# Kernel optimization log

Measured on AMD Instinct MI355X. Metric: run time of the kernel, lower is better.

The kernel has to match this reference:

```python
import jax, jax.numpy as jnp
import numpy as np

C = 64            # irrep multiplicity (64x0e + 64x1o)
N_BASIS = 8
N_SPECIES = 5
AVG_NEIGH = 16.0
CUTOFF = 5.0
N_PATHS = 5       # (0e*Y0->0e),(0e*Y1->1o),(1o*Y0->1o),(1o.Y1->0e),(1o x Y1->1)


def setup_inputs() -> dict:
    key = jax.random.key(0)
    ks = jax.random.split(key, 16)
    N, E = 20000, 320000
    def w(k, shape, fan_in):
        return jax.random.normal(k, shape, dtype=jnp.float32) / jnp.sqrt(jnp.float32(fan_in))
    return {
        "vectors": jax.random.normal(ks[0], (E, 3), dtype=jnp.float32),
        "node_feats": jax.random.normal(ks[1], (N, 4 * C), dtype=jnp.float32),
        "node_specie": jax.random.randint(ks[2], (N,), 0, N_SPECIES),
        "senders": jax.random.randint(ks[3], (E,), 0, N),
        "receivers": jax.random.randint(ks[4], (E,), 0, N),
        # linear_up (per-irrep channel mixing)
        "W0_up": w(ks[5], (C, C), C),
        "W1_up": w(ks[6], (C, C), C),
        # radial MLP: 8 -> 64 -> 64 -> 5*C
        "Wm1": w(ks[7], (N_BASIS, 64), N_BASIS),
        "Wm2": w(ks[8], (64, 64), 64),
        "Wm3": w(ks[9], (64, N_PATHS * C), 64),
        # skip_tp: species-indexed linear to 128x0e + 64x1o
        "Ws0": w(ks[10], (N_SPECIES, C, 2 * C), C),
        "Ws1": w(ks[11], (N_SPECIES, C, C), C),
        # linear_down: messages irreps -> 128x0e + 64x1o
        "Wd0": w(ks[12], (C, 2 * C), C),
        "Wd1": w(ks[13], (C, C), C),
    }


def reference(vectors, node_feats, node_specie, senders, receivers,
              W0_up, W1_up, Wm1, Wm2, Wm3, Ws0, Ws1, Wd0, Wd1):
    N = node_feats.shape[0]
    E = vectors.shape[0]
    x0 = node_feats[:, :C]                       # [N,C]   0e scalars
    x1 = node_feats[:, C:].reshape(N, C, 3)      # [N,C,3] 1o vectors

    # linear_up then gather by senders
    u0 = x0 @ W0_up
    u1 = jnp.einsum('nci,cd->ndi', x1, W1_up)
    m0 = u0[senders]                             # [E,C]
    m1 = u1[senders]                             # [E,C,3]

    # radial basis (bessel) and edge-weight MLP
    r = jnp.linalg.norm(vectors, axis=-1, keepdims=True)   # [E,1]
    safe_r = jnp.where(r == 0.0, 1.0, r)
    Y1 = vectors / safe_r                                  # [E,3] unit direction (l=1 SH)
    n = jnp.arange(1, N_BASIS + 1, dtype=vectors.dtype)
    basis = jnp.sqrt(2.0 / CUTOFF) * jnp.sin(n * jnp.pi * r / CUTOFF) / safe_r  # [E,8]
    h = jax.nn.silu(basis @ Wm1)
    h = jax.nn.silu(h @ Wm2)
    wmix = h @ Wm3                                         # [E, 5*C]
    wmix = jnp.where(r == 0.0, 0.0, wmix)                  # zero weights at zero-length edges
    w00, w01, w10, w11d, w11c = jnp.split(wmix, N_PATHS, axis=-1)  # each [E,C]

    # per-edge equivariant tensor product (LinearSHTP, l<=1 CG paths)
    dot = jnp.einsum('eci,ei->ec', m1, Y1)                 # 1o . Y1 -> scalar
    crs = jnp.cross(m1, Y1[:, None, :])                    # 1o x Y1 -> vector
    msg0 = w00 * m0 + w11d * dot                           # [E,C]
    msg1 = (w01 * m0)[..., None] * Y1[:, None, :] \
           + w10[..., None] * m1 + w11c[..., None] * crs   # [E,C,3]

    # scatter_sum to receivers, normalize by sqrt(avg_num_neighbors)
    inv = 1.0 / jnp.sqrt(jnp.float32(AVG_NEIGH))
    a0 = jax.ops.segment_sum(msg0, receivers, num_segments=N) * inv
    a1 = jax.ops.segment_sum(msg1.reshape(E, 3 * C), receivers, num_segments=N).reshape(N, C, 3) * inv

    # linear_down to 128x0e + 64x1o (extra 0e scalars are the gates)
    d0 = a0 @ Wd0                                          # [N,2C]
    d1 = jnp.einsum('nci,cd->ndi', a1, Wd1)                # [N,C,3]

    # skip_tp: species-indexed linear on original node features
    s0 = jnp.einsum('nc,ncd->nd', x0, Ws0[node_specie])    # [N,2C]
    s1 = jnp.einsum('nci,ncd->ndi', x1, Ws1[node_specie])  # [N,C,3]

    f0 = d0 + s0
    f1 = d1 + s1

    # gate: first C scalars -> even_act(silu); next C scalars gate the 1o vectors
    scalars = jax.nn.silu(f0[:, :C])
    gates = jax.nn.silu(f0[:, C:])
    vec = f1 * gates[..., None]
    return jnp.concatenate([scalars, vec.reshape(N, 3 * C)], axis=-1)  # [N, 4C]
```

## Files before the change

### kernel.cpp

```cpp
#include <hip/hip_runtime.h>
#include <hip/hip_bf16.h>

typedef __attribute__((ext_vector_type(8))) short short8;
typedef __attribute__((ext_vector_type(4))) float f32x4;
typedef __attribute__((ext_vector_type(4))) unsigned short us4v;

__device__ __forceinline__ unsigned bf16u(float x) {
    unsigned u = __float_as_uint(x);
    return (u + 0x7fffu + ((u >> 16) & 1u)) >> 16;
}
__device__ __forceinline__ short bf16s(float x) { return (short)bf16u(x); }

__global__ __launch_bounds__(256) void prep_kernel(
    const float* __restrict__ Wm1, const float* __restrict__ Wm2,
    const float* __restrict__ Wm3,
    const float* __restrict__ Wd0, const float* __restrict__ Ws0,
    const float* __restrict__ Wd1, const float* __restrict__ Ws1,
    short* __restrict__ W1B, short* __restrict__ Wm2B, short* __restrict__ W3B,
    short* __restrict__ WoB, int* __restrict__ cnt, int N)
{
    const int tid = blockIdx.x * 256 + threadIdx.x;
    const int nth = gridDim.x * 256;

    for (int i = tid; i < N * 16; i += nth) cnt[i] = 0;

    for (int idx = tid; idx < 52 * 64; idx += nth) {
        int l = idx & 63, f = idx >> 6;
        int g = l >> 4, c = l & 15;
        short8 v;
        if (f < 4) {
            #pragma unroll
            for (int i = 0; i < 8; ++i)
                v[i] = (g == 0) ? bf16s(Wm1[(size_t)i * 64 + f * 16 + c]) : (short)0;
            *(short8*)(W1B + (size_t)f * 512 + l * 8) = v;
        } else if (f < 12) {
            int f2 = f - 4, t = f2 >> 1, kh = f2 & 1;
            #pragma unroll
            for (int i = 0; i < 8; ++i)
                v[i] = bf16s(Wm2[(size_t)(kh * 32 + g * 8 + i) * 64 + t * 16 + c]);
            *(short8*)(Wm2B + (size_t)f2 * 512 + l * 8) = v;
        } else {
            int f3 = f - 12, t = f3 >> 1, kh = f3 & 1;
            #pragma unroll
            for (int i = 0; i < 8; ++i)
                v[i] = bf16s(Wm3[(size_t)(kh * 32 + g * 8 + i) * 320 + t * 16 + c]);
            *(short8*)(W3B + (size_t)f3 * 512 + l * 8) = v;
        }
    }

    for (int idx = tid; idx < 144 * 64; idx += nth) {
        int l = idx & 63, f = idx >> 6;
        int g = l >> 4, c = l & 15;
        short8 v;
        if (f < 16) {
            int t = f >> 1, kh = f & 1;
            #pragma unroll
            for (int i = 0; i < 8; ++i)
                v[i] = bf16s(Wd0[(size_t)(kh * 32 + g * 8 + i) * 128 + t * 16 + c]);
        } else if (f < 96) {
            int s = (f - 16) >> 4, r = (f - 16) & 15, t = r >> 1, kh = r & 1;
            #pragma unroll
            for (int i = 0; i < 8; ++i)
                v[i] = bf16s(Ws0[((size_t)s * 64 + kh * 32 + g * 8 + i) * 128 + t * 16 + c]);
        } else if (f < 104) {
            int r = f - 96, t = r >> 1, kh = r & 1;
            #pragma unroll
            for (int i = 0; i < 8; ++i)
                v[i] = bf16s(Wd1[(size_t)(kh * 32 + g * 8 + i) * 64 + t * 16 + c]);
        } else {
            int s = (f - 104) >> 3, r = (f - 104) & 7, t = r >> 1, kh = r & 1;
            #pragma unroll
            for (int i = 0; i < 8; ++i)
                v[i] = bf16s(Ws1[((size_t)s * 64 + kh * 32 + g * 8 + i) * 64 + t * 16 + c]);
        }
        *(short8*)(WoB + (size_t)f * 512 + l * 8) = v;
    }
}

__global__ __launch_bounds__(256) void rank_kernel(
    const int* __restrict__ receivers, int* __restrict__ cnt,
    int* __restrict__ rank, int E)
{
    int i = blockIdx.x * 256 + threadIdx.x;
    int stride = gridDim.x * 256;
    for (; i < E; i += stride)
        rank[i] = atomicAdd(&cnt[receivers[i] << 4], 1);
}

__global__ __launch_bounds__(256) void scan1_kernel(
    const int* __restrict__ cnt, int* __restrict__ offs,
    int* __restrict__ part, int N)
{
    __shared__ int a_[256], b_[256];
    const int b = blockIdx.x, t = threadIdx.x;
    const int base = b * 1024 + t * 4;
    int v[4];
    #pragma unroll
    for (int k = 0; k < 4; ++k)
        v[k] = (base + k < N) ? cnt[(size_t)(base + k) << 4] : 0;
    int sum = v[0] + v[1] + v[2] + v[3];
    a_[t] = sum;
    __syncthreads();
    int* src = a_; int* dst = b_;
    for (int off = 1; off < 256; off <<= 1) {
        dst[t] = src[t] + ((t >= off) ? src[t - off] : 0);
        __syncthreads();
        int* tmp = src; src = dst; dst = tmp;
    }
    int excl = src[t] - sum;
    if (t == 0) part[b] = src[255];
    int run = excl;
    #pragma unroll
    for (int k = 0; k < 4; ++k) {
        if (base + k < N) offs[base + k] = run;
        run += v[k];
    }
}

__global__ __launch_bounds__(256) void scan23_kernel(
    int* __restrict__ offs, const int* __restrict__ part, int nblk, int N)
{
    __shared__ int base_s, total_s;
    const int b = blockIdx.x, t = threadIdx.x;
    if (t == 0) {
        int s = 0, tot = 0;
        for (int i = 0; i < nblk; ++i) {
            if (i < b) s += part[i];
            tot += part[i];
        }
        base_s = s; total_s = tot;
    }
    __syncthreads();
    const int add = base_s;
    const int base = b * 1024 + t * 4;
    #pragma unroll
    for (int k = 0; k < 4; ++k) {
        int i = base + k;
        if (i < N) offs[i] += add;
    }
    if (b == 0 && t == 0) offs[N] = total_s;
}

__global__ __launch_bounds__(256) void fpnu_kernel(
    const float* __restrict__ vectors, const int* __restrict__ senders,
    const int* __restrict__ receivers, const int* __restrict__ offs,
    const int* __restrict__ rank,
    uint4* __restrict__ epackA, float4* __restrict__ epackB,
    const float* __restrict__ node_feats, const float* __restrict__ W0_up,
    const float* __restrict__ W1_up, uint2* __restrict__ ubf,
    short* __restrict__ xpk, int E, int N, int FPB)
{
    __shared__ float lnf[4][256];
    if (blockIdx.x < FPB) {
        int i = blockIdx.x * 256 + threadIdx.x;
        int stride = FPB * 256;
        for (; i < E; i += stride) {
            int pos = offs[receivers[i]] + rank[i];
            float vx = vectors[3 * (size_t)i + 0];
            float vy = vectors[3 * (size_t)i + 1];
            float vz = vectors[3 * (size_t)i + 2];
            float r = sqrtf(vx * vx + vy * vy + vz * vz);
            float ir = (r != 0.f) ? 1.f / r : 0.f;
            float ang = r * 0.6283185307179586f;
            float s1, c1;
            __sincosf(ang, &s1, &c1);
            float tc = 2.f * c1;
            float sb = s1, sp = 0.f;
            float coef = 0.6324555320336759f * ir;
            unsigned bw[4];
            #pragma unroll
            for (int h = 0; h < 4; ++h) {
                unsigned lo = bf16u(sb * coef);
                float nx = tc * sb - sp; sp = sb; sb = nx;
                unsigned hi = bf16u(sb * coef);
                nx = tc * sb - sp; sp = sb; sb = nx;
                bw[h] = lo | (hi << 16);
            }
            epackA[pos] = make_uint4(bw[0], bw[1], bw[2], bw[3]);
            epackB[pos] = make_float4(vx * ir, vy * ir, vz * ir,
                                      __int_as_float(senders[i]));
        }
    } else {
        const int wv = threadIdx.x >> 6;
        const int d  = threadIdx.x & 63;
        int nb = (blockIdx.x - FPB) * 4 + wv;
        if (nb >= N) return;

        float4 v4 = *(const float4*)(node_feats + (size_t)nb * 256 + d * 4);
        *(float4*)&lnf[wv][d * 4] = v4;

        float a0 = 0.f, ax = 0.f, ay = 0.f, az = 0.f;
        #pragma unroll 8
        for (int cc = 0; cc < 64; ++cc) {
            float w0 = W0_up[cc * 64 + d];
            float w1 = W1_up[cc * 64 + d];
            float x0v = lnf[wv][cc];
            float xxv = lnf[wv][64 + cc * 3 + 0];
            float xyv = lnf[wv][64 + cc * 3 + 1];
            float xzv = lnf[wv][64 + cc * 3 + 2];
            a0 += x0v * w0;
            ax += xxv * w1;
            ay += xyv * w1;
            az += xzv * w1;
        }
        ubf[(size_t)nb * 64 + d] = make_uint2(bf16u(a0) | (bf16u(ax) << 16),
                                              bf16u(ay) | (bf16u(az) << 16));
        short* xp = xpk + (size_t)nb * 256;
        xp[d]       = bf16s(lnf[wv][d]);
        xp[64 + d]  = bf16s(lnf[wv][64 + d * 3 + 0]);
        xp[128 + d] = bf16s(lnf[wv][64 + d * 3 + 1]);
        xp[192 + d] = bf16s(lnf[wv][64 + d * 3 + 2]);
    }
}

__global__ __launch_bounds__(256) void mlp_kernel(
    const uint4* __restrict__ epackA,
    const short* __restrict__ W1B, const short* __restrict__ Wm2B,
    const short* __restrict__ W3B, unsigned short* __restrict__ wmix,
    int P, int nwaves)
{
    __shared__ __align__(16) short ldsW3[40 * 512];
    __shared__ __align__(16) short ldsH[4][1024];

    {
        const short8* src = (const short8*)W3B;
        short8* dst = (short8*)ldsW3;
        for (int i = threadIdx.x; i < 2560; i += 256) dst[i] = src[i];
    }
    __syncthreads();

    const int lane = threadIdx.x & 63;
    const int wv   = threadIdx.x >> 6;
    const int gw   = blockIdx.x * 4 + wv;
    const int c = lane & 15, g = lane >> 4;
    const int nwin = (P + 15) >> 4;

    for (int w = gw; w < nwin; w += nwaves) {
        const int p0 = w << 4;

        short8 basisA = {0, 0, 0, 0, 0, 0, 0, 0};
        if (lane < 16) {
            uint4 ba = epackA[p0 + lane];
            union { uint4 u4v; short8 s8; } cv;
            cv.u4v = ba;
            basisA = cv.s8;
        }

        #pragma unroll
        for (int t = 0; t < 4; ++t) {
            f32x4 h = {0.f, 0.f, 0.f, 0.f};
            short8 bf = *(const short8*)(W1B + (size_t)t * 512 + lane * 8);
            h = __builtin_amdgcn_mfma_f32_16x16x32_bf16(basisA, bf, h, 0, 0, 0);
            #pragma unroll
            for (int i = 0; i < 4; ++i) {
                float x = h[i];
                float h1 = x / (1.f + __expf(-x));
                int row = 4 * g + i;
                ldsH[wv][row * 64 + ((16 * t + c) ^ ((row & 7) << 3))] = bf16s(h1);
            }
        }
        short8 h1f0 = *(const short8*)&ldsH[wv][c * 64 + ((g * 8) ^ ((c & 7) << 3))];
        short8 h1f1 = *(const short8*)&ldsH[wv][c * 64 + ((32 + g * 8) ^ ((c & 7) << 3))];

        #pragma unroll
        for (int t = 0; t < 4; ++t) {
            f32x4 h = {0.f, 0.f, 0.f, 0.f};
            short8 b0 = *(const short8*)(Wm2B + (size_t)(t * 2) * 512 + lane * 8);
            short8 b1 = *(const short8*)(Wm2B + (size_t)(t * 2 + 1) * 512 + lane * 8);
            h = __builtin_amdgcn_mfma_f32_16x16x32_bf16(h1f0, b0, h, 0, 0, 0);
            h = __builtin_amdgcn_mfma_f32_16x16x32_bf16(h1f1, b1, h, 0, 0, 0);
            #pragma unroll
            for (int i = 0; i < 4; ++i) {
                float x = h[i];
                float h2 = x / (1.f + __expf(-x));
                int row = 4 * g + i;
                ldsH[wv][row * 64 + ((16 * t + c) ^ ((row & 7) << 3))] = bf16s(h2);
            }
        }
        short8 h2f0 = *(const short8*)&ldsH[wv][c * 64 + ((g * 8) ^ ((c & 7) << 3))];
        short8 h2f1 = *(const short8*)&ldsH[wv][c * 64 + ((32 + g * 8) ^ ((c & 7) << 3))];

        unsigned short* wbase = wmix + (size_t)w * 5120 + lane * 4;
        #pragma unroll
        for (int t = 0; t < 20; ++t) {
            f32x4 wq = {0.f, 0.f, 0.f, 0.f};
            short8 b0 = *(const short8*)(ldsW3 + (size_t)(t * 2) * 512 + lane * 8);
            short8 b1 = *(const short8*)(ldsW3 + (size_t)(t * 2 + 1) * 512 + lane * 8);
            wq = __builtin_amdgcn_mfma_f32_16x16x32_bf16(h2f0, b0, wq, 0, 0, 0);
            wq = __builtin_amdgcn_mfma_f32_16x16x32_bf16(h2f1, b1, wq, 0, 0, 0);
            us4v st;
            #pragma unroll
            for (int i = 0; i < 4; ++i) st[i] = (unsigned short)bf16u(wq[i]);
            *(us4v*)(wbase + t * 256) = st;
        }
    }
}

__global__ __launch_bounds__(256) void gather_kernel(
    const float4* __restrict__ epackB, const int* __restrict__ offs,
    const uint2* __restrict__ ubf, const unsigned short* __restrict__ wmix,
    float* __restrict__ acc, int N)
{
    const int lane = threadIdx.x & 63;
    const int n = blockIdx.x * 4 + (threadIdx.x >> 6);
    if (n >= N) return;
    const int q = lane >> 4, c = lane & 15;

    const int beg = offs[n], end = offs[n + 1];
    float a0 = 0.f, a1x = 0.f, a1y = 0.f, a1z = 0.f;

    for (int base = beg & ~3; base < end; base += 4) {
        const unsigned short* wn = wmix
            + (size_t)(base >> 4) * 5120
            + (q << 8) + (((base & 15) >> 2) << 6) + (c << 2);
        us4v wp0 = *(const us4v*)(wn);
        us4v wp1 = *(const us4v*)(wn + 1024);
        us4v wp2 = *(const us4v*)(wn + 2048);
        us4v wp3 = *(const us4v*)(wn + 3072);
        us4v wp4 = *(const us4v*)(wn + 4096);

        #pragma unroll
        for (int i = 0; i < 4; ++i) {
            int pos = base + i;
            bool valid = (pos >= beg) && (pos < end);
            float4 mb = epackB[pos];
            int snd = valid ? __float_as_int(mb.w) : 0;
            uint2 mu = ubf[(size_t)snd * 64 + lane];
            float w00  = valid ? __uint_as_float((unsigned)wp0[i] << 16) : 0.f;
            float w01  = valid ? __uint_as_float((unsigned)wp1[i] << 16) : 0.f;
            float w10  = valid ? __uint_as_float((unsigned)wp2[i] << 16) : 0.f;
            float w11d = valid ? __uint_as_float((unsigned)wp3[i] << 16) : 0.f;
            float w11c = valid ? __uint_as_float((unsigned)wp4[i] << 16) : 0.f;
            float m0  = __uint_as_float(mu.x << 16);
            float m1x = __uint_as_float(mu.x & 0xffff0000u);
            float m1y = __uint_as_float(mu.y << 16);
            float m1z = __uint_as_float(mu.y & 0xffff0000u);

            float dotv = m1x * mb.x + m1y * mb.y + m1z * mb.z;
            a0 += w00 * m0 + w11d * dotv;
            float wm = w01 * m0;
            a1x += wm * mb.x + w10 * m1x + w11c * (m1y * mb.z - m1z * mb.y);
            a1y += wm * mb.y + w10 * m1y + w11c * (m1z * mb.x - m1x * mb.z);
            a1z += wm * mb.z + w10 * m1z + w11c * (m1x * mb.y - m1y * mb.x);
        }
    }

    float* ar = acc + (size_t)n * 256;
    ar[lane]       = a0;
    ar[64 + lane]  = a1x;
    ar[128 + lane] = a1y;
    ar[192 + lane] = a1z;
}

__global__ __launch_bounds__(256) void edge_kernel(
    const uint4* __restrict__ epackA, const float4* __restrict__ epackB,
    const int* __restrict__ offs, const uint2* __restrict__ ubf,
    const short* __restrict__ W1B, const short* __restrict__ Wm2B,
    const short* __restrict__ W3B, float* __restrict__ acc,
    int N, int nwaves)
{
    __shared__ __align__(16) short ldsW3[40 * 512];
    __shared__ __align__(16) short ldsH[4][1024];
    __shared__ __align__(16) float ldsMeta[4][16][4];

    {
        const short8* src = (const short8*)W3B;
        short8* dst = (short8*)ldsW3;
        for (int i = threadIdx.x; i < 2560; i += 256) dst[i] = src[i];
    }
    __syncthreads();

    const int lane = threadIdx.x & 63;
    const int wv   = threadIdx.x >> 6;
    const int gw   = blockIdx.x * 4 + wv;
    const int c = lane & 15, g = lane >> 4;

    for (int n = gw; n < N; n += nwaves) {
        float a0q[4]  = {0.f, 0.f, 0.f, 0.f};
        float a1xq[4] = {0.f, 0.f, 0.f, 0.f};
        float a1yq[4] = {0.f, 0.f, 0.f, 0.f};
        float a1zq[4] = {0.f, 0.f, 0.f, 0.f};
        const int beg = offs[n], end = offs[n + 1];

        for (int p0 = beg; p0 < end; p0 += 16) {
            const int m = end - p0;
            short8 basisA = {0, 0, 0, 0, 0, 0, 0, 0};
            if (lane < 16) {
                uint4 ba = epackA[p0 + lane];
                float4 mb = epackB[p0 + lane];
                if (lane >= m) {
                    ba = make_uint4(0u, 0u, 0u, 0u);
                    mb = make_float4(0.f, 0.f, 0.f, __int_as_float(0));
                }
                union { uint4 u4v; short8 s8; } cv;
                cv.u4v = ba;
                basisA = cv.s8;
                *(float4*)&ldsMeta[wv][lane][0] = mb;
            }
            float Yx[4], Yy[4], Yz[4];
            int snd[4];
            #pragma unroll
            for (int i = 0; i < 4; ++i) {
                float4 mt = *(const float4*)&ldsMeta[wv][4 * g + i][0];
                Yx[i] = mt.x; Yy[i] = mt.y; Yz[i] = mt.z;
                snd[i] = __float_as_int(mt.w);
            }

#define PFETCH(Q, MV)                                                       \
            _Pragma("unroll")                                               \
            for (int i = 0; i < 4; ++i)                                     \
                MV[i] = ubf[(size_t)snd[i] * 64 + 16 * (Q) + c];

#define COMPQ(Q, MV)                                                        \
        {                                                                   \
            float M0[4], M1X[4], M1Y[4], M1Z[4];                            \
            _Pragma("unroll")                                               \
            for (int i = 0; i < 4; ++i) {                                   \
                M0[i]  = __uint_as_float(MV[i].x << 16);                    \
                M1X[i] = __uint_as_float(MV[i].x & 0xffff0000u);            \
                M1Y[i] = __uint_as_float(MV[i].y << 16);                    \
                M1Z[i] = __uint_as_float(MV[i].y & 0xffff0000u);            \
            }                                                               \
            _Pragma("unroll")                                               \
            for (int p = 0; p < 5; ++p) {                                   \
                const int t = 4 * p + (Q);                                  \
                f32x4 w = {0.f, 0.f, 0.f, 0.f};                             \
                short8 b0 = *(const short8*)(ldsW3 + (size_t)(t * 2) * 512 + lane * 8);     \
                short8 b1 = *(const short8*)(ldsW3 + (size_t)(t * 2 + 1) * 512 + lane * 8); \
                w = __builtin_amdgcn_mfma_f32_16x16x32_bf16(h2f0, b0, w, 0, 0, 0);          \
                w = __builtin_amdgcn_mfma_f32_16x16x32_bf16(h2f1, b1, w, 0, 0, 0);          \
                _Pragma("unroll")                                           \
                for (int i = 0; i < 4; ++i) {                               \
                    float wv_ = w[i];                                       \
                    if (p == 0) {                                           \
                        a0q[Q] += wv_ * M0[i];                              \
                    } else if (p == 1) {                                    \
                        float tt = wv_ * M0[i];                             \
                        a1xq[Q] += tt * Yx[i];                              \
                        a1yq[Q] += tt * Yy[i];                              \
                        a1zq[Q] += tt * Yz[i];                              \
                    } else if (p == 2) {                                    \
                        a1xq[Q] += wv_ * M1X[i];                            \
                        a1yq[Q] += wv_ * M1Y[i];                            \
                        a1zq[Q] += wv_ * M1Z[i];                            \
                    } else if (p == 3) {                                    \
                        a0q[Q] += wv_ * (M1X[i] * Yx[i] + M1Y[i] * Yy[i] + M1Z[i] * Yz[i]); \
                    } else {                                                \
                        a1xq[Q] += wv_ * (M1Y[i] * Yz[i] - M1Z[i] * Yy[i]); \
                        a1yq[Q] += wv_ * (M1Z[i] * Yx[i] - M1X[i] * Yz[i]); \
                        a1zq[Q] += wv_ * (M1X[i] * Yy[i] - M1Y[i] * Yx[i]); \
                    }                                                       \
                }                                                           \
            }                                                               \
        }

            uint2 mA[4], mB[4];
            PFETCH(0, mA);
            PFETCH(1, mB);
            __builtin_amdgcn_sched_barrier(0);

            #pragma unroll
            for (int t = 0; t < 4; ++t) {
                f32x4 h = {0.f, 0.f, 0.f, 0.f};
                short8 bf = *(const short8*)(W1B + (size_t)t * 512 + lane * 8);
                h = __builtin_amdgcn_mfma_f32_16x16x32_bf16(basisA, bf, h, 0, 0, 0);
                #pragma unroll
                for (int i = 0; i < 4; ++i) {
                    float x = h[i];
                    float h1 = x / (1.f + __expf(-x));
                    int row = 4 * g + i;
                    ldsH[wv][row * 64 + ((16 * t + c) ^ ((row & 7) << 3))] = bf16s(h1);
                }
            }
            short8 h1f0 = *(const short8*)&ldsH[wv][c * 64 + ((g * 8) ^ ((c & 7) << 3))];
            short8 h1f1 = *(const short8*)&ldsH[wv][c * 64 + ((32 + g * 8) ^ ((c & 7) << 3))];

            #pragma unroll
            for (int t = 0; t < 4; ++t) {
                f32x4 h = {0.f, 0.f, 0.f, 0.f};
                short8 b0 = *(const short8*)(Wm2B + (size_t)(t * 2) * 512 + lane * 8);
                short8 b1 = *(const short8*)(Wm2B + (size_t)(t * 2 + 1) * 512 + lane * 8);
                h = __builtin_amdgcn_mfma_f32_16x16x32_bf16(h1f0, b0, h, 0, 0, 0);
                h = __builtin_amdgcn_mfma_f32_16x16x32_bf16(h1f1, b1, h, 0, 0, 0);
                #pragma unroll
                for (int i = 0; i < 4; ++i) {
                    float x = h[i];
                    float h2 = x / (1.f + __expf(-x));
                    int row = 4 * g + i;
                    ldsH[wv][row * 64 + ((16 * t + c) ^ ((row & 7) << 3))] = bf16s(h2);
                }
            }
            short8 h2f0 = *(const short8*)&ldsH[wv][c * 64 + ((g * 8) ^ ((c & 7) << 3))];
            short8 h2f1 = *(const short8*)&ldsH[wv][c * 64 + ((32 + g * 8) ^ ((c & 7) << 3))];

            COMPQ(0, mA);
            __builtin_amdgcn_sched_barrier(0);
            PFETCH(2, mA);
            COMPQ(1, mB);
            __builtin_amdgcn_sched_barrier(0);
            PFETCH(3, mB);
            COMPQ(2, mA);
            __builtin_amdgcn_sched_barrier(0);
            COMPQ(3, mB);
#undef PFETCH
#undef COMPQ
        }

        #pragma unroll
        for (int q = 0; q < 4; ++q) {
            a0q[q]  += __shfl_xor(a0q[q], 16);  a0q[q]  += __shfl_xor(a0q[q], 32);
            a1xq[q] += __shfl_xor(a1xq[q], 16); a1xq[q] += __shfl_xor(a1xq[q], 32);
            a1yq[q] += __shfl_xor(a1yq[q], 16); a1yq[q] += __shfl_xor(a1yq[q], 32);
            a1zq[q] += __shfl_xor(a1zq[q], 16); a1zq[q] += __shfl_xor(a1zq[q], 32);
        }
        if (lane < 16) {
            float* ar = acc + (size_t)n * 256;
            #pragma unroll
            for (int q = 0; q < 4; ++q) {
                ar[16 * q + lane]       = a0q[q];
                ar[64 + 16 * q + lane]  = a1xq[q];
                ar[128 + 16 * q + lane] = a1yq[q];
                ar[192 + 16 * q + lane] = a1zq[q];
            }
        }
    }
}

__global__ __launch_bounds__(256) void node_out_kernel(
    const float* __restrict__ acc, const short* __restrict__ xpk,
    const int* __restrict__ node_specie, const short* __restrict__ WoB,
    float* __restrict__ out, int N)
{
    __shared__ float ldsOut[4][16][256];
    const int lane = threadIdx.x & 63;
    const int wv   = threadIdx.x >> 6;
    const int c = lane & 15, g = lane >> 4;
    const int n0 = (blockIdx.x * 4 + wv) * 16;
    if (n0 >= N) return;

    const int nc = min(n0 + c, N - 1);
    const int sp_c = node_specie[nc];
    const short8 z8 = {0, 0, 0, 0, 0, 0, 0, 0};

    short8 x0f[2], a0hi[2], a0lo[2];
    #pragma unroll
    for (int kh = 0; kh < 2; ++kh) {
        x0f[kh] = *(const short8*)&xpk[(size_t)nc * 256 + kh * 32 + g * 8];
        const float* ap = acc + (size_t)nc * 256 + kh * 32 + g * 8;
        #pragma unroll
        for (int i = 0; i < 8; ++i) {
            float v = 0.25f * ap[i];
            unsigned h = bf16u(v);
            a0hi[kh][i] = (short)h;
            a0lo[kh][i] = (short)bf16u(v - __uint_as_float(h << 16));
        }
    }

    f32x4 w0[8];
    #pragma unroll
    for (int t = 0; t < 8; ++t) w0[t] = (f32x4){0.f, 0.f, 0.f, 0.f};
    #pragma unroll
    for (int t = 0; t < 8; ++t)
        #pragma unroll
        for (int kh = 0; kh < 2; ++kh) {
            short8 b = *(const short8*)(WoB + (size_t)(t * 2 + kh) * 512 + lane * 8);
            w0[t] = __builtin_amdgcn_mfma_f32_16x16x32_bf16(a0hi[kh], b, w0[t], 0, 0, 0);
            w0[t] = __builtin_amdgcn_mfma_f32_16x16x32_bf16(a0lo[kh], b, w0[t], 0, 0, 0);
        }
    #pragma unroll
    for (int s = 0; s < 5; ++s) {
        if (!__any(sp_c == s)) continue;
        short8 mk0 = (sp_c == s) ? x0f[0] : z8;
        short8 mk1 = (sp_c == s) ? x0f[1] : z8;
        #pragma unroll
        for (int t = 0; t < 8; ++t) {
            short8 b0 = *(const short8*)(WoB + (size_t)(16 + s * 16 + t * 2) * 512 + lane * 8);
            short8 b1 = *(const short8*)(WoB + (size_t)(16 + s * 16 + t * 2 + 1) * 512 + lane * 8);
            w0[t] = __builtin_amdgcn_mfma_f32_16x16x32_bf16(mk0, b0, w0[t], 0, 0, 0);
            w0[t] = __builtin_amdgcn_mfma_f32_16x16x32_bf16(mk1, b1, w0[t], 0, 0, 0);
        }
    }
    float gate[4][4];
    #pragma unroll
    for (int t = 0; t < 8; ++t)
        #pragma unroll
        for (int i = 0; i < 4; ++i) {
            float x = w0[t][i];
            float sv = x / (1.f + __expf(-x));
            if (t < 4) ldsOut[wv][4 * g + i][16 * t + c] = sv;
            else       gate[t - 4][i] = sv;
        }

    short8 x1f[3][2], a1hi[3][2], a1lo[3][2];
    #pragma unroll
    for (int j = 0; j < 3; ++j)
        #pragma unroll
        for (int kh = 0; kh < 2; ++kh) {
            x1f[j][kh] = *(const short8*)&xpk[(size_t)nc * 256 + (1 + j) * 64 + kh * 32 + g * 8];
            const float* ap = acc + (size_t)nc * 256 + 64 + 64 * j + kh * 32 + g * 8;
            #pragma unroll
            for (int i = 0; i < 8; ++i) {
                float v = 0.25f * ap[i];
                unsigned h = bf16u(v);
                a1hi[j][kh][i] = (short)h;
                a1lo[j][kh][i] = (short)bf16u(v - __uint_as_float(h << 16));
            }
        }

    f32x4 w1[3][4];
    #pragma unroll
    for (int j = 0; j < 3; ++j)
        #pragma unroll
        for (int t = 0; t < 4; ++t) w1[j][t] = (f32x4){0.f, 0.f, 0.f, 0.f};
    #pragma unroll
    for (int t = 0; t < 4; ++t)
        #pragma unroll
        for (int kh = 0; kh < 2; ++kh) {
            short8 b = *(const short8*)(WoB + (size_t)(96 + t * 2 + kh) * 512 + lane * 8);
            #pragma unroll
            for (int j = 0; j < 3; ++j) {
                w1[j][t] = __builtin_amdgcn_mfma_f32_16x16x32_bf16(a1hi[j][kh], b, w1[j][t], 0, 0, 0);
                w1[j][t] = __builtin_amdgcn_mfma_f32_16x16x32_bf16(a1lo[j][kh], b, w1[j][t], 0, 0, 0);
            }
        }
    #pragma unroll
    for (int s = 0; s < 5; ++s) {
        if (!__any(sp_c == s)) continue;
        short8 m1[3][2];
        #pragma unroll
        for (int j = 0; j < 3; ++j) {
            m1[j][0] = (sp_c == s) ? x1f[j][0] : z8;
            m1[j][1] = (sp_c == s) ? x1f[j][1] : z8;
        }
        #pragma unroll
        for (int t = 0; t < 4; ++t)
            #pragma unroll
            for (int kh = 0; kh < 2; ++kh) {
                short8 b = *(const short8*)(WoB + (size_t)(104 + s * 8 + t * 2 + kh) * 512 + lane * 8);
                #pragma unroll
                for (int j = 0; j < 3; ++j)
                    w1[j][t] = __builtin_amdgcn_mfma_f32_16x16x32_bf16(m1[j][kh], b, w1[j][t], 0, 0, 0);
            }
    }
    #pragma unroll
    for (int j = 0; j < 3; ++j)
        #pragma unroll
        for (int t = 0; t < 4; ++t)
            #pragma unroll
            for (int i = 0; i < 4; ++i)
                ldsOut[wv][4 * g + i][64 + (16 * t + c) * 3 + j] = w1[j][t][i] * gate[t][i];

    #pragma unroll 4
    for (int r = 0; r < 16; ++r) {
        int nn = n0 + r;
        if (nn < N)
            *(float4*)&out[(size_t)nn * 256 + lane * 4] =
                *(const float4*)&ldsOut[wv][r][lane * 4];
    }
}

extern "C" void kernel_launch(void* const* d_in, const int* in_sizes, int n_in,
                              void* d_out, int out_size, void* d_ws, size_t ws_size,
                              hipStream_t stream) {
    const float* vectors     = (const float*)d_in[0];
    const float* node_feats  = (const float*)d_in[1];
    const int*   node_specie = (const int*)d_in[2];
    const int*   senders     = (const int*)d_in[3];
    const int*   receivers   = (const int*)d_in[4];
    const float* W0_up       = (const float*)d_in[5];
    const float* W1_up       = (const float*)d_in[6];
    const float* Wm1         = (const float*)d_in[7];
    const float* Wm2         = (const float*)d_in[8];
    const float* Wm3         = (const float*)d_in[9];
    const float* Ws0         = (const float*)d_in[10];
    const float* Ws1         = (const float*)d_in[11];
    const float* Wd0         = (const float*)d_in[12];
    const float* Wd1         = (const float*)d_in[13];
    float* out = (float*)d_out;

    int E = in_sizes[0] / 3;
    int N = in_sizes[1] / 256;
    int nblk = (N + 1023) / 1024;

    char* wp = (char*)d_ws;
    uint2* ubf     = (uint2*)wp;                wp += (size_t)N * 64 * 8;
    float* acc     = (float*)wp;                wp += (size_t)N * 256 * 4;
    short* xpk     = (short*)wp;                wp += (size_t)N * 256 * 2;
    uint4* epackA  = (uint4*)wp;                wp += (size_t)(E + 16) * 16;
    float4* epackB = (float4*)wp;               wp += (size_t)(E + 16) * 16;
    unsigned short* wmix = (unsigned short*)wp;
    size_t wmix_bytes = (size_t)(E + 16) * 320 * 2;
    size_t base_used = (size_t)(wp - (char*)d_ws);
    size_t other_bytes = (4 + 8 + 40 + 144) * 512 * 2
                       + (size_t)N * 16 * 4
                       + (size_t)(N + 1) * 4
                       + (size_t)E * 4
                       + (size_t)(nblk + 1) * 4 + 256;
    bool use_split = (base_used + wmix_bytes + other_bytes) <= ws_size;
    if (use_split) wp += wmix_bytes;

    short* W1B    = (short*)wp;                 wp += 4 * 512 * 2;
    short* Wm2B   = (short*)wp;                 wp += 8 * 512 * 2;
    short* W3B    = (short*)wp;                 wp += 40 * 512 * 2;
    short* WoB    = (short*)wp;                 wp += 144 * 512 * 2;
    int*   cnt    = (int*)wp;                   wp += (size_t)N * 16 * 4;
    int*   offs   = (int*)wp;                   wp += (size_t)(N + 1) * 4;
    int*   rank   = (int*)wp;                   wp += (size_t)E * 4;
    int*   part   = (int*)wp;                   wp += (size_t)(nblk + 1) * 4;

    prep_kernel<<<80, 256, 0, stream>>>(
        Wm1, Wm2, Wm3, Wd0, Ws0, Wd1, Ws1, W1B, Wm2B, W3B, WoB, cnt, N);
    rank_kernel<<<1024, 256, 0, stream>>>(receivers, cnt, rank, E);
    scan1_kernel<<<nblk, 256, 0, stream>>>(cnt, offs, part, N);
    scan23_kernel<<<nblk, 256, 0, stream>>>(offs, part, nblk, N);
    const int FPB = 1024;
    fpnu_kernel<<<FPB + (N + 3) / 4, 256, 0, stream>>>(
        vectors, senders, receivers, offs, rank, epackA, epackB,
        node_feats, W0_up, W1_up, ubf, xpk, E, N, FPB);

    if (use_split) {
        mlp_kernel<<<768, 256, 0, stream>>>(
            epackA, W1B, Wm2B, W3B, wmix, E, 768 * 4);
        gather_kernel<<<(N + 3) / 4, 256, 0, stream>>>(
            epackB, offs, ubf, wmix, acc, N);
    } else {
        edge_kernel<<<512, 256, 0, stream>>>(
            epackA, epackB, offs, ubf, W1B, Wm2B, W3B, acc, N, 512 * 4);
    }

    int ngroups = (N + 15) / 16;
    node_out_kernel<<<(ngroups + 3) / 4, 256, 0, stream>>>(
        acc, xpk, node_specie, WoB, out, N);
}
```

Baseline: 205.1 us.

## Pad per-node edge segments to multiples of four for aligned gather

The CSR scan now rounds each node's degree up to a multiple of 4, so every node's edge segment starts on a 4-aligned position. The gather loop can start at beg directly and drops the lower-bound validity check, and the end is taken from the real count. The MLP reads the padded total from the device instead of using E, and the edge buffers grow by up to 3N entries. The trade-off is extra MLP work on padding slots, more memory, and reliance on the padding entries being harmless (they are masked by the valid check).

```diff
diff --git a/kernel.cpp b/kernel.cpp
--- a/kernel.cpp
+++ b/kernel.cpp
@@ -96,8 +96,10 @@
     const int base = b * 1024 + t * 4;
     int v[4];
     #pragma unroll
-    for (int k = 0; k < 4; ++k)
-        v[k] = (base + k < N) ? cnt[(size_t)(base + k) << 4] : 0;
+    for (int k = 0; k < 4; ++k) {
+        int d = (base + k < N) ? cnt[(size_t)(base + k) << 4] : 0;
+        v[k] = (d + 3) & ~3;
+    }
     int sum = v[0] + v[1] + v[2] + v[3];
     a_[t] = sum;
     __syncthreads();
@@ -214,10 +216,10 @@
 }
 
 __global__ __launch_bounds__(256) void mlp_kernel(
-    const uint4* __restrict__ epackA,
+    const uint4* __restrict__ epackA, const int* __restrict__ totalp,
     const short* __restrict__ W1B, const short* __restrict__ Wm2B,
     const short* __restrict__ W3B, unsigned short* __restrict__ wmix,
-    int P, int nwaves)
+    int nwaves)
 {
     __shared__ __align__(16) short ldsW3[40 * 512];
     __shared__ __align__(16) short ldsH[4][1024];
@@ -229,6 +231,7 @@
     }
     __syncthreads();
 
+    const int P = *totalp;
     const int lane = threadIdx.x & 63;
     const int wv   = threadIdx.x >> 6;
     const int gw   = blockIdx.x * 4 + wv;
@@ -298,6 +301,7 @@
 
 __global__ __launch_bounds__(256) void gather_kernel(
     const float4* __restrict__ epackB, const int* __restrict__ offs,
+    const int* __restrict__ cnt,
     const uint2* __restrict__ ubf, const unsigned short* __restrict__ wmix,
     float* __restrict__ acc, int N)
 {
@@ -306,10 +310,12 @@
     if (n >= N) return;
     const int q = lane >> 4, c = lane & 15;
 
-    const int beg = offs[n], end = offs[n + 1];
+    const int beg = offs[n];
+    const int deg = cnt[(size_t)n << 4];
+    const int end = beg + deg;
     float a0 = 0.f, a1x = 0.f, a1y = 0.f, a1z = 0.f;
 
-    for (int base = beg & ~3; base < end; base += 4) {
+    for (int base = beg; base < end; base += 4) {
         const unsigned short* wn = wmix
             + (size_t)(base >> 4) * 5120
             + (q << 8) + (((base & 15) >> 2) << 6) + (c << 2);
@@ -322,7 +328,7 @@
         #pragma unroll
         for (int i = 0; i < 4; ++i) {
             int pos = base + i;
-            bool valid = (pos >= beg) && (pos < end);
+            bool valid = (pos < end);
             float4 mb = epackB[pos];
             int snd = valid ? __float_as_int(mb.w) : 0;
             uint2 mu = ubf[(size_t)snd * 64 + lane];
@@ -354,7 +360,8 @@
 
 __global__ __launch_bounds__(256) void edge_kernel(
     const uint4* __restrict__ epackA, const float4* __restrict__ epackB,
-    const int* __restrict__ offs, const uint2* __restrict__ ubf,
+    const int* __restrict__ offs, const int* __restrict__ cnt,
+    const uint2* __restrict__ ubf,
     const short* __restrict__ W1B, const short* __restrict__ Wm2B,
     const short* __restrict__ W3B, float* __restrict__ acc,
     int N, int nwaves)
@@ -380,7 +387,8 @@
         float a1xq[4] = {0.f, 0.f, 0.f, 0.f};
         float a1yq[4] = {0.f, 0.f, 0.f, 0.f};
         float a1zq[4] = {0.f, 0.f, 0.f, 0.f};
-        const int beg = offs[n], end = offs[n + 1];
+        const int beg = offs[n];
+        const int end = beg + cnt[(size_t)n << 4];
 
         for (int p0 = beg; p0 < end; p0 += 16) {
             const int m = end - p0;
@@ -681,15 +689,16 @@
     int E = in_sizes[0] / 3;
     int N = in_sizes[1] / 256;
     int nblk = (N + 1023) / 1024;
+    size_t EP = (size_t)E + 3 * (size_t)N + 32;
 
     char* wp = (char*)d_ws;
     uint2* ubf     = (uint2*)wp;                wp += (size_t)N * 64 * 8;
     float* acc     = (float*)wp;                wp += (size_t)N * 256 * 4;
     short* xpk     = (short*)wp;                wp += (size_t)N * 256 * 2;
-    uint4* epackA  = (uint4*)wp;                wp += (size_t)(E + 16) * 16;
-    float4* epackB = (float4*)wp;               wp += (size_t)(E + 16) * 16;
+    uint4* epackA  = (uint4*)wp;                wp += EP * 16;
+    float4* epackB = (float4*)wp;               wp += EP * 16;
     unsigned short* wmix = (unsigned short*)wp;
-    size_t wmix_bytes = (size_t)(E + 16) * 320 * 2;
+    size_t wmix_bytes = EP * 320 * 2;
     size_t base_used = (size_t)(wp - (char*)d_ws);
     size_t other_bytes = (4 + 8 + 40 + 144) * 512 * 2
                        + (size_t)N * 16 * 4
@@ -720,12 +729,12 @@
 
     if (use_split) {
         mlp_kernel<<<768, 256, 0, stream>>>(
-            epackA, W1B, Wm2B, W3B, wmix, E, 768 * 4);
+            epackA, offs + N, W1B, Wm2B, W3B, wmix, 768 * 4);
         gather_kernel<<<(N + 3) / 4, 256, 0, stream>>>(
-            epackB, offs, ubf, wmix, acc, N);
+            epackB, offs, cnt, ubf, wmix, acc, N);
     } else {
         edge_kernel<<<512, 256, 0, stream>>>(
-            epackA, epackB, offs, ubf, W1B, Wm2B, W3B, acc, N, 512 * 4);
+            epackA, epackB, offs, cnt, ubf, W1B, Wm2B, W3B, acc, N, 512 * 4);
     }
 
     int ngroups = (N + 15) / 16;
```

New measurement: 219.5 us. +7.0%, slower.
